# Kernel optimization log

Hardware: AMD Instinct MI355X
Metric: run time of the kernel (lower is better)

The kernel has to match this reference:

```python
import jax, jax.numpy as jnp
import numpy as np

B, T, D = 2, 2048, 4096
H, G, d = 32, 8, 128
GROUP = H // G  # 4


def setup_inputs() -> dict:
    key = jax.random.key(0)
    ks = jax.random.split(key, 9)
    s = 0.02
    return {
        "hidden_states": jax.random.normal(ks[0], (B, T, D), jnp.float32),
        "Wq": jax.random.normal(ks[1], (D, D), jnp.float32) * s,
        "bq": jax.random.normal(ks[2], (D,), jnp.float32) * s,
        "Wk": jax.random.normal(ks[3], (G * d, D), jnp.float32) * s,
        "bk": jax.random.normal(ks[4], (G * d,), jnp.float32) * s,
        "Wv": jax.random.normal(ks[5], (G * d, D), jnp.float32) * s,
        "bv": jax.random.normal(ks[6], (G * d,), jnp.float32) * s,
        "Wo": jax.random.normal(ks[7], (D, D), jnp.float32) * s,
        "bo": jax.random.normal(ks[8], (D,), jnp.float32) * s,
    }


def reference(hidden_states, Wq, bq, Wk, bk, Wv, bv, Wo, bo):
    # projections (torch Linear: x @ W.T + b)
    q = hidden_states @ Wq.T + bq            # [B,T,D]
    k = hidden_states @ Wk.T + bk            # [B,T,G*d]
    v = hidden_states @ Wv.T + bv            # [B,T,G*d]

    # [B,G,group,T,d] for q; [B,G,T,d] for k,v. repeat_interleave(group, dim=1)
    # on [B,H,...] is exactly the (G, group) grouping of heads.
    q = q.reshape(B, T, G, GROUP, d).transpose(0, 2, 3, 1, 4)  # bgptd
    k = k.reshape(B, T, G, d).transpose(0, 2, 1, 3)            # bgsd
    v = v.reshape(B, T, G, d).transpose(0, 2, 1, 3)            # bgsd

    scale = 1.0 / np.sqrt(d).astype(np.float32)
    scores = jnp.einsum("bgptd,bgsd->bgpts", q, k) * scale     # [B,G,group,Tq,Tk]

    # causal additive mask: (j > i) * -1e9  (past_len = 0)
    i = jnp.arange(T)[:, None]
    j = jnp.arange(T)[None, :]
    causal_add = (j > i).astype(scores.dtype) * -1e9
    scores = scores + causal_add               # broadcast over b,g,p

    attn = jax.nn.softmax(scores, axis=-1)
    y = jnp.einsum("bgpts,bgsd->bgptd", attn, v)               # [B,G,group,T,d]
    y = y.transpose(0, 3, 1, 2, 4).reshape(B, T, D)            # [B,T,H*d]
    return y @ Wo.T + bo
```

## Files before the change

### kernel.cpp

```cpp
#include <hip/hip_runtime.h>
#include <hip/hip_bf16.h>
#include <cstdint>
#include <cstddef>

using bf16 = __hip_bfloat16;
typedef __attribute__((ext_vector_type(8))) short bf16x8;
typedef __attribute__((ext_vector_type(4))) float floatx4;

#define GLOBAL_AS __attribute__((address_space(1)))
#define LDS_AS    __attribute__((address_space(3)))

__device__ __forceinline__ void async_copy16(void* lds, const void* g) {
    __builtin_amdgcn_global_load_lds((GLOBAL_AS void*)(g), (LDS_AS void*)(lds), 16, 0, 0);
}

__device__ __forceinline__ floatx4 mfma_bf16(bf16x8 a, bf16x8 b, floatx4 c) {
    return __builtin_amdgcn_mfma_f32_16x16x32_bf16(a, b, c, 0, 0, 0);
}

__global__ void cvt_f32_bf16(const float* __restrict__ src, bf16* __restrict__ dst, int n) {
    int i = (blockIdx.x * blockDim.x + threadIdx.x) * 4;
    if (i < n) {
        float4 v = *(const float4*)(src + i);
        __align__(8) bf16 t[4];
        t[0] = __float2bfloat16(v.x);
        t[1] = __float2bfloat16(v.y);
        t[2] = __float2bfloat16(v.z);
        t[3] = __float2bfloat16(v.w);
        *(short4*)(dst + i) = *(const short4*)t;
    }
}

#define MMBLK(AF, MB, NB) do {                                                 \
    __builtin_amdgcn_s_setprio(1);                                             \
    _Pragma("unroll") for (int kk = 0; kk < 2; ++kk)                           \
    _Pragma("unroll") for (int mi = 0; mi < 4; ++mi)                           \
    _Pragma("unroll") for (int ni = 0; ni < 2; ++ni)                           \
        acc[(MB) + mi][(NB) + ni] =                                            \
            mfma_bf16(AF[mi][kk], bb[ni][kk], acc[(MB) + mi][(NB) + ni]);      \
    __builtin_amdgcn_s_setprio(0);                                             \
} while (0)

#define BAR()   __builtin_amdgcn_s_barrier()
#define LGKM0() asm volatile("s_waitcnt lgkmcnt(0)" ::: "memory")
#define VM4()   asm volatile("s_waitcnt vmcnt(4)" ::: "memory")
#define VM0()   asm volatile("s_waitcnt vmcnt(0)" ::: "memory")

template <int OUTF>
__global__ __launch_bounds__(512, 2) void gemm256_bt_bias(
    const bf16* __restrict__ A, const bf16* __restrict__ W,
    const float* __restrict__ bias, void* __restrict__ Cv,
    int M, int N, int K, float cscale)
{
    __shared__ __align__(16) bf16 sA[2][2][128 * 64];
    __shared__ __align__(16) bf16 sB[2][2][128 * 64];

    const int tid  = threadIdx.x;
    const int lane = tid & 63;
    const int wave = tid >> 6;
    const int quad = lane >> 4;
    const int l16  = lane & 15;
    const int wmi  = wave >> 2;
    const int wni  = wave & 3;

    const int bm = blockIdx.x;
    const int bn = blockIdx.y;

    const int srow = tid >> 3;
    const int sc16 = tid & 7;

    auto STAGE = [&](bf16* dst, const bf16* G, int rowbase, int kt) {
#pragma unroll
        for (int i = 0; i < 2; ++i) {
            const int row = i * 64 + srow;
            async_copy16(dst + (i * 512 + tid) * 8,
                         G + (size_t)(rowbase + row) * K + kt * 64 + ((sc16 ^ (row & 7)) * 8));
        }
    };
    auto LDA = [&](int bi, int mi, int kk) -> bf16x8 {
        const bf16* base = &sA[bi][wmi][0];
        const int r = mi * 16 + l16;
        return *(const bf16x8*)(base + r * 64 + (((kk * 4 + quad) ^ (r & 7)) * 8));
    };
    auto LDB = [&](int bi, int ni, int kk) -> bf16x8 {
        const bf16* base = &sB[bi][wni >> 1][0];
        const int r = (wni & 1) * 64 + ni * 16 + l16;
        return *(const bf16x8*)(base + r * 64 + (((kk * 4 + quad) ^ (r & 7)) * 8));
    };

    floatx4 acc[8][4];
#pragma unroll
    for (int i = 0; i < 8; ++i)
#pragma unroll
        for (int j = 0; j < 4; ++j) acc[i][j] = (floatx4){0.f, 0.f, 0.f, 0.f};

    const int rowA = bm * 256;
    const int rowB = bn * 256;
    const int iters = K >> 7;

    STAGE(&sA[0][0][0], A, rowA + 0,   0);
    STAGE(&sA[0][1][0], A, rowA + 128, 0);
    STAGE(&sB[0][0][0], W, rowB + 0,   0);
    STAGE(&sB[0][1][0], W, rowB + 128, 0);
    STAGE(&sA[1][0][0], A, rowA + 0,   1);
    STAGE(&sA[1][1][0], A, rowA + 128, 1);
    VM4();
    BAR();

    bf16x8 a0[4][2], a1[4][2], bb[2][2];
    for (int i = 0; i < iters; ++i) {
        const int kt = 2 * i;
        const bool nl = (i + 1 < iters);

#pragma unroll
        for (int mi = 0; mi < 4; ++mi) { a0[mi][0] = LDA(0, mi, 0); a0[mi][1] = LDA(0, mi, 1); }
#pragma unroll
        for (int ni = 0; ni < 2; ++ni) { bb[ni][0] = LDB(0, ni, 0); bb[ni][1] = LDB(0, ni, 1); }
        STAGE(&sB[1][0][0], W, rowB + 0, kt + 1);
        BAR(); LGKM0();
        MMBLK(a0, 0, 0);
        BAR();
#pragma unroll
        for (int mi = 0; mi < 4; ++mi) { a1[mi][0] = LDA(0, mi + 4, 0); a1[mi][1] = LDA(0, mi + 4, 1); }
        STAGE(&sB[1][1][0], W, rowB + 128, kt + 1);
        BAR(); LGKM0();
        MMBLK(a1, 4, 0);
        BAR();
#pragma unroll
        for (int ni = 0; ni < 2; ++ni) { bb[ni][0] = LDB(0, ni + 2, 0); bb[ni][1] = LDB(0, ni + 2, 1); }
        if (nl) STAGE(&sA[0][0][0], A, rowA + 0, kt + 2);
        BAR(); LGKM0();
        MMBLK(a0, 0, 2);
        BAR();
        if (nl) { STAGE(&sA[0][1][0], A, rowA + 128, kt + 2); VM4(); }
        else    { VM0(); }
        BAR();
        MMBLK(a1, 4, 2);
        BAR();
#pragma unroll
        for (int mi = 0; mi < 4; ++mi) { a0[mi][0] = LDA(1, mi, 0); a0[mi][1] = LDA(1, mi, 1); }
#pragma unroll
        for (int ni = 0; ni < 2; ++ni) { bb[ni][0] = LDB(1, ni, 0); bb[ni][1] = LDB(1, ni, 1); }
        if (nl) STAGE(&sB[0][0][0], W, rowB + 0, kt + 2);
        BAR(); LGKM0();
        MMBLK(a0, 0, 0);
        BAR();
#pragma unroll
        for (int mi = 0; mi < 4; ++mi) { a1[mi][0] = LDA(1, mi + 4, 0); a1[mi][1] = LDA(1, mi + 4, 1); }
        if (nl) STAGE(&sB[0][1][0], W, rowB + 128, kt + 2);
        BAR(); LGKM0();
        MMBLK(a1, 4, 0);
        BAR();
#pragma unroll
        for (int ni = 0; ni < 2; ++ni) { bb[ni][0] = LDB(1, ni + 2, 0); bb[ni][1] = LDB(1, ni + 2, 1); }
        if (nl) STAGE(&sA[1][0][0], A, rowA + 0, kt + 3);
        BAR(); LGKM0();
        MMBLK(a0, 0, 2);
        BAR();
        if (nl) { STAGE(&sA[1][1][0], A, rowA + 128, kt + 3); VM4(); }
        BAR();
        MMBLK(a1, 4, 2);
        BAR();
    }

#pragma unroll
    for (int mi = 0; mi < 8; ++mi) {
        const int row0 = bm * 256 + wmi * 128 + mi * 16 + quad * 4;
#pragma unroll
        for (int ni = 0; ni < 4; ++ni) {
            const int col = bn * 256 + wni * 64 + ni * 16 + l16;
            const float bv = bias[col];
            if (OUTF) {
                float* C = (float*)Cv;
#pragma unroll
                for (int r = 0; r < 4; ++r)
                    C[(size_t)(row0 + r) * N + col] = (acc[mi][ni][r] + bv) * cscale;
            } else {
                bf16* C = (bf16*)Cv;
#pragma unroll
                for (int r = 0; r < 4; ++r)
                    C[(size_t)(row0 + r) * N + col] = __float2bfloat16((acc[mi][ni][r] + bv) * cscale);
            }
        }
    }
}

__global__ __launch_bounds__(256, 3) void gemm_kv(
    const bf16* __restrict__ A,
    const bf16* __restrict__ Wk, const bf16* __restrict__ Wv,
    const float* __restrict__ bk, const float* __restrict__ bv,
    bf16* __restrict__ kout, bf16* __restrict__ vt,
    int M, int K)
{
    __shared__ __align__(16) bf16 As[128 * 32];
    __shared__ __align__(16) bf16 Ws[128 * 32];

    const int tid  = threadIdx.x;
    const int lane = tid & 63;
    const int wave = tid >> 6;
    const int quad = lane >> 4;
    const int l16  = lane & 15;
    const int wm = (wave >> 1) * 64;
    const int wn = (wave & 1) * 64;

    const int bm = blockIdx.x;
    const int bn = blockIdx.y;
    const bool isK = (bn < 8);
    const int nb = isK ? bn : (bn - 8);
    const bf16* Wsel  = isK ? Wk : Wv;
    const float* bsel = isK ? bk : bv;

    floatx4 acc[4][4];
#pragma unroll
    for (int i = 0; i < 4; ++i)
#pragma unroll
        for (int j = 0; j < 4; ++j) acc[i][j] = (floatx4){0.f, 0.f, 0.f, 0.f};

    const int srow = tid >> 2;
    const int scol = (tid & 3) * 8;
    const bf16* gA = A    + (size_t)(bm * 128 + srow) * K + scol;
    const bf16* gW = Wsel + (size_t)(nb * 128 + srow) * K + scol;
    bf16* lA0 = As + tid * 8;
    bf16* lA1 = As + 2048 + tid * 8;
    bf16* lW0 = Ws + tid * 8;
    bf16* lW1 = Ws + 2048 + tid * 8;
    const size_t skip = (size_t)64 * K;

    const int kt_n = K >> 5;
    for (int kt = 0; kt < kt_n; ++kt) {
        __syncthreads();
        const bf16* ga = gA + kt * 32;
        const bf16* gw = gW + kt * 32;
        async_copy16(lA0, ga);
        async_copy16(lA1, ga + skip);
        async_copy16(lW0, gw);
        async_copy16(lW1, gw + skip);
        __syncthreads();

        bf16x8 af[4], bfr[4];
#pragma unroll
        for (int mi = 0; mi < 4; ++mi)
            af[mi] = *(const bf16x8*)(As + (wm + mi * 16 + l16) * 32 + quad * 8);
#pragma unroll
        for (int ni = 0; ni < 4; ++ni)
            bfr[ni] = *(const bf16x8*)(Ws + (wn + ni * 16 + l16) * 32 + quad * 8);
#pragma unroll
        for (int mi = 0; mi < 4; ++mi)
#pragma unroll
            for (int ni = 0; ni < 4; ++ni)
                acc[mi][ni] = mfma_bf16(af[mi], bfr[ni], acc[mi][ni]);
    }

#pragma unroll
    for (int mi = 0; mi < 4; ++mi) {
        const int row0 = bm * 128 + wm + mi * 16 + quad * 4;
#pragma unroll
        for (int ni = 0; ni < 4; ++ni) {
            const int col = nb * 128 + wn + ni * 16 + l16;
            const float bvv = bsel[col];
            if (isK) {
#pragma unroll
                for (int r = 0; r < 4; ++r)
                    kout[(size_t)(row0 + r) * 1024 + col] = __float2bfloat16(acc[mi][ni][r] + bvv);
            } else {
                __align__(8) bf16 tmp[4];
#pragma unroll
                for (int r = 0; r < 4; ++r) tmp[r] = __float2bfloat16(acc[mi][ni][r] + bvv);
                const int b  = row0 >> 11;
                const int t0 = row0 & 2047;
                bf16* dst = vt + ((size_t)(b * 1024 + col)) * 2048 + t0;
                *(short4*)dst = *(const short4*)tmp;
            }
        }
    }
}

__global__ __launch_bounds__(256, 2) void attn_fwd(
    const bf16* __restrict__ qb, const bf16* __restrict__ kb,
    const bf16* __restrict__ vtb, bf16* __restrict__ ob)
{
    constexpr int T  = 2048;
    constexpr int DQ = 4096;
    constexpr int DK = 1024;

    __shared__ __align__(16) bf16 Ks[2][64 * 128];
    __shared__ __align__(16) bf16 Vs[2][128 * 64];
    __shared__ __align__(16) bf16 Ps[4][16][72];

    const int tid  = threadIdx.x;
    const int lane = tid & 63;
    const int wave = tid >> 6;
    const int quad = lane >> 4;
    const int l16  = lane & 15;
    const int swz  = l16 & 7;

    const int qi = blockIdx.x;
    const int bh = blockIdx.y;
    const int b  = bh >> 5;
    const int h  = bh & 31;
    const int g  = h >> 2;
    const int qtB = 31 - qi;
    const int qtA = qi;
    const int q0B = qtB * 64;
    const int q0A = qtA * 64;
    const int qw = wave * 16;

    const bf16* Qg = qb  + (size_t)b * T * DQ + (size_t)h * 128;
    const bf16* Kg = kb  + (size_t)b * T * DK + (size_t)g * 128;
    const bf16* Vg = vtb + ((size_t)b * DK + g * 128) * T;
    bf16*       Og = ob  + (size_t)b * T * DQ + (size_t)h * 128;

    bf16x8 qf[2][4];
    {
        const size_t rB = (size_t)(q0B + qw + l16) * DQ;
        const size_t rA = (size_t)(q0A + qw + l16) * DQ;
#pragma unroll
        for (int kk = 0; kk < 4; ++kk) {
            qf[0][kk] = *(const bf16x8*)(Qg + rB + kk * 32 + quad * 8);
            qf[1][kk] = *(const bf16x8*)(Qg + rA + kk * 32 + quad * 8);
        }
    }

    const int krow_l = tid >> 4;
    const int kc16   = tid & 15;
    const int vrow_l = tid >> 3;
    const int vc16   = tid & 7;

    auto STAGE = [&](int st_, int bi_) {
        const int s0_ = st_ * 64;
        bf16* kbp = &Ks[bi_][0];
        bf16* vbp = &Vs[bi_][0];
#pragma unroll
        for (int i = 0; i < 4; ++i) {
            const int r = i * 16 + krow_l;
            async_copy16(kbp + (i * 256 + tid) * 8,
                         Kg + (size_t)(s0_ + r) * DK + ((kc16 ^ (r & 7)) * 8));
        }
#pragma unroll
        for (int i = 0; i < 4; ++i) {
            const int r = i * 32 + vrow_l;
            async_copy16(vbp + (i * 256 + tid) * 8,
                         Vg + (size_t)r * T + s0_ + ((vc16 ^ (r & 7)) * 8));
        }
    };

    floatx4 oacc[2][8];
#pragma unroll
    for (int t = 0; t < 2; ++t)
#pragma unroll
        for (int i = 0; i < 8; ++i) oacc[t][i] = (floatx4){0.f, 0.f, 0.f, 0.f};
    float m_run[2], l_run[2];
#pragma unroll
    for (int t = 0; t < 2; ++t) { m_run[t] = -1e30f; l_run[t] = 0.f; }

    const int bsrc = (lane & 48) + quad * 4;

    STAGE(0, 0);
    __syncthreads();

    for (int st = 0; st <= qtB; ++st) {
        const int bi = st & 1;
        const int s0 = st * 64;

        if (st < qtB) STAGE(st + 1, bi ^ 1);

        const bf16* Kb = &Ks[bi][0];
        const bf16* Vb = &Vs[bi][0];

        const int ntile = (st <= qtA) ? 2 : 1;
#pragma unroll
        for (int t = 0; t < 2; ++t) {
            if (t >= ntile) break;
            const int q0t  = t ? q0A : q0B;
            const int qt_t = t ? qtA : qtB;

            floatx4 sacc[4];
#pragma unroll
            for (int i = 0; i < 4; ++i) sacc[i] = (floatx4){0.f, 0.f, 0.f, 0.f};
#pragma unroll
            for (int kk = 0; kk < 4; ++kk) {
                const int koff = ((kk * 4 + quad) ^ swz) * 8;
                const bf16x8 qv = qf[t][kk];
#pragma unroll
                for (int ni = 0; ni < 4; ++ni) {
                    bf16x8 kf = *(const bf16x8*)(Kb + (ni * 16 + l16) * 128 + koff);
                    sacc[ni] = mfma_bf16(kf, qv, sacc[ni]);
                }
            }

            const bool diag = (st == qt_t);
            const int qg = q0t + qw + l16;
            float sv[4][4];
#pragma unroll
            for (int ni = 0; ni < 4; ++ni)
#pragma unroll
                for (int r = 0; r < 4; ++r) {
                    float x = sacc[ni][r];
                    if (diag && (s0 + ni * 16 + quad * 4 + r) > qg) x = -1e30f;
                    sv[ni][r] = x;
                }

            float pm[4];
#pragma unroll
            for (int ni = 0; ni < 4; ++ni)
                pm[ni] = fmaxf(fmaxf(sv[ni][0], sv[ni][1]), fmaxf(sv[ni][2], sv[ni][3]));
            float mx = fmaxf(fmaxf(pm[0], pm[1]), fmaxf(pm[2], pm[3]));
            mx = fmaxf(mx, __shfl_xor(mx, 16, 64));
            mx = fmaxf(mx, __shfl_xor(mx, 32, 64));

            const float mold  = m_run[t];
            const float mnew  = fmaxf(mold, mx);
            const float alpha = __expf(mold - mnew);
            m_run[t] = mnew;

            float ssum = 0.f;
#pragma unroll
            for (int ni = 0; ni < 4; ++ni) {
                __align__(8) bf16 pb[4];
#pragma unroll
                for (int r = 0; r < 4; ++r) {
                    float p = __expf(sv[ni][r] - mnew);
                    ssum += p;
                    pb[r] = __float2bfloat16(p);
                }
                *(short4*)&Ps[wave][l16][ni * 16 + quad * 4] = *(const short4*)pb;
            }
            ssum += __shfl_xor(ssum, 16, 64);
            ssum += __shfl_xor(ssum, 32, 64);
            l_run[t] = l_run[t] * alpha + ssum;

            float ar[4];
#pragma unroll
            for (int r = 0; r < 4; ++r) ar[r] = __shfl(alpha, bsrc + r, 64);
#pragma unroll
            for (int db = 0; db < 8; ++db)
#pragma unroll
                for (int r = 0; r < 4; ++r) oacc[t][db][r] *= ar[r];

            asm volatile("s_waitcnt lgkmcnt(0)" ::: "memory");

#pragma unroll
            for (int kk = 0; kk < 2; ++kk) {
                bf16x8 ap = *(const bf16x8*)&Ps[wave][l16][kk * 32 + quad * 8];
                const int voff = ((kk * 4 + quad) ^ swz) * 8;
#pragma unroll
                for (int db = 0; db < 8; ++db) {
                    bf16x8 bv8 = *(const bf16x8*)(Vb + (db * 16 + l16) * 64 + voff);
                    oacc[t][db] = mfma_bf16(ap, bv8, oacc[t][db]);
                }
            }
        }

        __syncthreads();
    }

#pragma unroll
    for (int t = 0; t < 2; ++t) {
        const int q0t = t ? q0A : q0B;
        const float linv = 1.0f / l_run[t];
        float ir[4];
#pragma unroll
        for (int r = 0; r < 4; ++r) ir[r] = __shfl(linv, bsrc + r, 64);
#pragma unroll
        for (int r = 0; r < 4; ++r) {
            const int qg = q0t + qw + quad * 4 + r;
#pragma unroll
            for (int db = 0; db < 8; ++db)
                Og[(size_t)qg * DQ + db * 16 + l16] = __float2bfloat16(oacc[t][db][r] * ir[r]);
        }
    }
}

extern "C" void kernel_launch(void* const* d_in, const int* in_sizes, int n_in,
                              void* d_out, int out_size, void* d_ws, size_t ws_size,
                              hipStream_t stream)
{
    const float* hs = (const float*)d_in[0];
    const float* Wq = (const float*)d_in[1];
    const float* bq = (const float*)d_in[2];
    const float* Wk = (const float*)d_in[3];
    const float* bk = (const float*)d_in[4];
    const float* Wv = (const float*)d_in[5];
    const float* bv = (const float*)d_in[6];
    const float* Wo = (const float*)d_in[7];
    const float* bo = (const float*)d_in[8];
    float* out = (float*)d_out;

    const int M  = 4096;
    const int D  = 4096;
    const int DK = 1024;
    const size_t SZ_D  = (size_t)M * D;
    const size_t SZ_K  = (size_t)M * DK;

    bf16* hsb  = (bf16*)d_ws;
    bf16* Wqb  = hsb  + SZ_D;
    bf16* Wkb  = Wqb  + SZ_D;
    bf16* Wvb  = Wkb  + SZ_K;
    bf16* Wob  = Wvb  + SZ_K;
    bf16* q_buf = Wob + SZ_D;
    bf16* k_buf = q_buf + SZ_D;
    bf16* vt_buf = Wqb;
    bf16* o_buf  = hsb;

    const int CB = 256;
    cvt_f32_bf16<<<(int)(SZ_D / 4 + CB - 1) / CB, CB, 0, stream>>>(hs, hsb, (int)SZ_D);
    cvt_f32_bf16<<<(int)(SZ_D / 4 + CB - 1) / CB, CB, 0, stream>>>(Wq, Wqb, (int)SZ_D);
    cvt_f32_bf16<<<(int)(SZ_K / 4 + CB - 1) / CB, CB, 0, stream>>>(Wk, Wkb, (int)SZ_K);
    cvt_f32_bf16<<<(int)(SZ_K / 4 + CB - 1) / CB, CB, 0, stream>>>(Wv, Wvb, (int)SZ_K);
    cvt_f32_bf16<<<(int)(SZ_D / 4 + CB - 1) / CB, CB, 0, stream>>>(Wo, Wob, (int)SZ_D);

    const float scale = 0.08838834764831845f;
    gemm256_bt_bias<0><<<dim3(M / 256, D / 256), dim3(512), 0, stream>>>(hsb, Wqb, bq, q_buf, M, D, D, scale);
    gemm_kv<<<dim3(M / 128, 16), dim3(256), 0, stream>>>(hsb, Wkb, Wvb, bk, bv, k_buf, vt_buf, M, D);
    attn_fwd<<<dim3(16, 64), dim3(256), 0, stream>>>(q_buf, k_buf, vt_buf, o_buf);
    gemm256_bt_bias<1><<<dim3(M / 256, D / 256), dim3(512), 0, stream>>>(o_buf, Wob, bo, out, M, D, D, 1.0f);
}
```

Baseline: 746.1 us.

## Software-pipeline LDS fragment reads and swizzle block order in GEMM

Restructures the GEMM main loop so A and B register fragments are double-buffered (b01/b23) and LDS reads for the next MFMA block are issued before the current block runs. Partial lgkmcnt waits replace full drains, and the MFMA order is changed so more B fragments get reused. It also remaps block IDs into eight interleaved groups, likely so concurrently running blocks share tiles in cache across XCDs. The cost is higher register pressure, and the hand-counted waitcnt values are error-prone.

```diff
diff --git a/kernel.cpp b/kernel.cpp
--- a/kernel.cpp
+++ b/kernel.cpp
@@ -31,20 +31,34 @@
     }
 }
 
-#define MMBLK(AF, MB, NB) do {                                                 \
+#define MMBLK(AF, BF, MB, NB) do {                                             \
     __builtin_amdgcn_s_setprio(1);                                             \
     _Pragma("unroll") for (int kk = 0; kk < 2; ++kk)                           \
     _Pragma("unroll") for (int mi = 0; mi < 4; ++mi)                           \
     _Pragma("unroll") for (int ni = 0; ni < 2; ++ni)                           \
         acc[(MB) + mi][(NB) + ni] =                                            \
-            mfma_bf16(AF[mi][kk], bb[ni][kk], acc[(MB) + mi][(NB) + ni]);      \
+            mfma_bf16(AF[mi][kk], BF[ni][kk], acc[(MB) + mi][(NB) + ni]);      \
     __builtin_amdgcn_s_setprio(0);                                             \
 } while (0)
 
-#define BAR()   __builtin_amdgcn_s_barrier()
-#define LGKM0() asm volatile("s_waitcnt lgkmcnt(0)" ::: "memory")
-#define VM4()   asm volatile("s_waitcnt vmcnt(4)" ::: "memory")
-#define VM0()   asm volatile("s_waitcnt vmcnt(0)" ::: "memory")
+#define READ_A(DST, BI, H) do {                                                \
+    _Pragma("unroll") for (int mi = 0; mi < 4; ++mi) {                         \
+        DST[mi][0] = LDA(BI, (H) * 4 + mi, 0);                                 \
+        DST[mi][1] = LDA(BI, (H) * 4 + mi, 1);                                 \
+    }                                                                          \
+} while (0)
+
+#define READ_B(DST, BI, P) do {                                                \
+    _Pragma("unroll") for (int ni = 0; ni < 2; ++ni) {                         \
+        DST[ni][0] = LDB(BI, (P) * 2 + ni, 0);                                 \
+        DST[ni][1] = LDB(BI, (P) * 2 + ni, 1);                                 \
+    }                                                                          \
+} while (0)
+
+#define BAR()    __builtin_amdgcn_s_barrier()
+#define LGKM(N)  asm volatile("s_waitcnt lgkmcnt(" #N ")" ::: "memory")
+#define VM4()    asm volatile("s_waitcnt vmcnt(4)" ::: "memory")
+#define VM0()    asm volatile("s_waitcnt vmcnt(0)" ::: "memory")
 
 template <int OUTF>
 __global__ __launch_bounds__(512, 2) void gemm256_bt_bias(
@@ -63,8 +77,12 @@
     const int wmi  = wave >> 2;
     const int wni  = wave & 3;
 
-    const int bm = blockIdx.x;
-    const int bn = blockIdx.y;
+    const int nbx  = gridDim.x;
+    const int bidl = blockIdx.y * nbx + blockIdx.x;
+    const int cpx  = (nbx * gridDim.y) >> 3;
+    const int sid  = (bidl & 7) * cpx + (bidl >> 3);
+    const int bm   = sid % nbx;
+    const int bn   = sid / nbx;
 
     const int srow = tid >> 3;
     const int sc16 = tid & 7;
@@ -107,59 +125,60 @@
     VM4();
     BAR();
 
-    bf16x8 a0[4][2], a1[4][2], bb[2][2];
+    bf16x8 a0[4][2], a1[4][2], b01[2][2], b23[2][2];
+    READ_A(a0, 0, 0);
+    READ_B(b01, 0, 0);
+
     for (int i = 0; i < iters; ++i) {
         const int kt = 2 * i;
         const bool nl = (i + 1 < iters);
 
-#pragma unroll
-        for (int mi = 0; mi < 4; ++mi) { a0[mi][0] = LDA(0, mi, 0); a0[mi][1] = LDA(0, mi, 1); }
-#pragma unroll
-        for (int ni = 0; ni < 2; ++ni) { bb[ni][0] = LDB(0, ni, 0); bb[ni][1] = LDB(0, ni, 1); }
+        READ_B(b23, 0, 1);
         STAGE(&sB[1][0][0], W, rowB + 0, kt + 1);
-        BAR(); LGKM0();
-        MMBLK(a0, 0, 0);
-        BAR();
-#pragma unroll
-        for (int mi = 0; mi < 4; ++mi) { a1[mi][0] = LDA(0, mi + 4, 0); a1[mi][1] = LDA(0, mi + 4, 1); }
+        BAR(); LGKM(4);
+        MMBLK(a0, b01, 0, 0);
+        BAR();
+        READ_A(a1, 0, 1);
         STAGE(&sB[1][1][0], W, rowB + 128, kt + 1);
-        BAR(); LGKM0();
-        MMBLK(a1, 4, 0);
-        BAR();
-#pragma unroll
-        for (int ni = 0; ni < 2; ++ni) { bb[ni][0] = LDB(0, ni + 2, 0); bb[ni][1] = LDB(0, ni + 2, 1); }
+        BAR(); LGKM(8);
+        MMBLK(a0, b23, 0, 2);
+        BAR();
+        LGKM(0);
         if (nl) STAGE(&sA[0][0][0], A, rowA + 0, kt + 2);
-        BAR(); LGKM0();
-        MMBLK(a0, 0, 2);
+        BAR();
+        MMBLK(a1, b01, 4, 0);
         BAR();
         if (nl) { STAGE(&sA[0][1][0], A, rowA + 128, kt + 2); VM4(); }
         else    { VM0(); }
         BAR();
-        MMBLK(a1, 4, 2);
-        BAR();
-#pragma unroll
-        for (int mi = 0; mi < 4; ++mi) { a0[mi][0] = LDA(1, mi, 0); a0[mi][1] = LDA(1, mi, 1); }
-#pragma unroll
-        for (int ni = 0; ni < 2; ++ni) { bb[ni][0] = LDB(1, ni, 0); bb[ni][1] = LDB(1, ni, 1); }
+        READ_A(a0, 1, 0);
+        READ_B(b01, 1, 0);
+        LGKM(12);
+        MMBLK(a1, b23, 4, 2);
+        BAR();
+        READ_B(b23, 1, 1);
         if (nl) STAGE(&sB[0][0][0], W, rowB + 0, kt + 2);
-        BAR(); LGKM0();
-        MMBLK(a0, 0, 0);
-        BAR();
-#pragma unroll
-        for (int mi = 0; mi < 4; ++mi) { a1[mi][0] = LDA(1, mi + 4, 0); a1[mi][1] = LDA(1, mi + 4, 1); }
+        BAR(); LGKM(4);
+        MMBLK(a0, b01, 0, 0);
+        BAR();
+        READ_A(a1, 1, 1);
         if (nl) STAGE(&sB[0][1][0], W, rowB + 128, kt + 2);
-        BAR(); LGKM0();
-        MMBLK(a1, 4, 0);
-        BAR();
-#pragma unroll
-        for (int ni = 0; ni < 2; ++ni) { bb[ni][0] = LDB(1, ni + 2, 0); bb[ni][1] = LDB(1, ni + 2, 1); }
+        BAR(); LGKM(8);
+        MMBLK(a0, b23, 0, 2);
+        BAR();
+        LGKM(0);
         if (nl) STAGE(&sA[1][0][0], A, rowA + 0, kt + 3);
-        BAR(); LGKM0();
-        MMBLK(a0, 0, 2);
+        BAR();
+        MMBLK(a1, b01, 4, 0);
         BAR();
         if (nl) { STAGE(&sA[1][1][0], A, rowA + 128, kt + 3); VM4(); }
         BAR();
-        MMBLK(a1, 4, 2);
+        if (nl) {
+            READ_A(a0, 0, 0);
+            READ_B(b01, 0, 0);
+            LGKM(12);
+        }
+        MMBLK(a1, b23, 4, 2);
         BAR();
     }
 
```

New measurement: 971.6 us. 30.2% more time.
